# Optimization experiments

Measured on AMD Instinct MI355X. Metric: run time of the kernel, lower is better.

## Reference

```python
import jax, jax.numpy as jnp
import numpy as np

N = 100_000      # nodes (10kb Hi-C bins)
E = 3_200_000    # edges (avg degree 32)
IN = 6           # histone-mark features
HID1 = 6
HID2 = 30
HEADS = 4
NEG_SLOPE = 0.2  # PyG GATConv default LeakyReLU slope


def setup_inputs() -> dict:
    key = jax.random.key(0)
    ks = jax.random.split(key, 16)
    def glorot(k, shape, fan_in):
        return (jax.random.normal(k, shape, jnp.float32) / np.float32(np.sqrt(fan_in)))
    x = jax.random.normal(ks[0], (N, IN), jnp.float32)
    edge_index = jax.random.randint(ks[1], (2, E), 0, N, dtype=jnp.int32)
    edge_attr = jax.random.uniform(ks[2], (E,), jnp.float32)  # ignored (edge_dim=None)
    # GATConv 1: IN -> HID1, HEADS, concat=True
    w1 = glorot(ks[3], (IN, HEADS * HID1), IN)
    att_src1 = glorot(ks[4], (HEADS, HID1), HID1)
    att_dst1 = glorot(ks[5], (HEADS, HID1), HID1)
    b1 = jnp.zeros((HEADS * HID1,), jnp.float32)
    # GATConv 2: HEADS*HID1 -> HID2, HEADS, concat=False (head mean)
    w2 = glorot(ks[6], (HEADS * HID1, HEADS * HID2), HEADS * HID1)
    att_src2 = glorot(ks[7], (HEADS, HID2), HID2)
    att_dst2 = glorot(ks[8], (HEADS, HID2), HID2)
    b2 = jnp.zeros((HID2,), jnp.float32)
    # MLP head
    ffw1 = glorot(ks[9], (HID2, HID2 // 2), HID2)
    ffb1 = jnp.zeros((HID2 // 2,), jnp.float32)
    ffw2 = glorot(ks[10], (HID2 // 2, 2), HID2 // 2)
    ffb2 = jnp.zeros((2,), jnp.float32)
    return {"x": x, "edge_index": edge_index, "edge_attr": edge_attr,
            "w1": w1, "att_src1": att_src1, "att_dst1": att_dst1, "b1": b1,
            "w2": w2, "att_src2": att_src2, "att_dst2": att_dst2, "b2": b2,
            "ffw1": ffw1, "ffb1": ffb1, "ffw2": ffw2, "ffb2": ffb2}


def _leaky(z):
    return jnp.where(z > 0, z, NEG_SLOPE * z)


def _gat_conv(x, src, dst, W, a_src, a_dst, b, heads, ch, concat):
    n = x.shape[0]
    h = (x @ W).reshape(n, heads, ch)                       # [N,H,C]
    asrc = jnp.einsum('nhc,hc->nh', h, a_src)               # [N,H]
    adst = jnp.einsum('nhc,hc->nh', h, a_dst)               # [N,H]
    e = _leaky(asrc[src] + adst[dst])                       # [E,H]
    # stable segment softmax over incoming edges of each dst node
    m = jax.ops.segment_max(e, dst, num_segments=n)
    e = jnp.exp(e - m[dst])
    denom = jax.ops.segment_sum(e, dst, num_segments=n)
    alpha = e / (denom[dst] + 1e-16)                        # [E,H]
    msg = h[src] * alpha[:, :, None]                        # [E,H,C]
    out = jax.ops.segment_sum(msg, dst, num_segments=n)     # [N,H,C]
    out = out.reshape(n, heads * ch) if concat else out.mean(axis=1)
    return out + b


def reference(x, edge_index, edge_attr, w1, att_src1, att_dst1, b1,
              w2, att_src2, att_dst2, b2, ffw1, ffb1, ffw2, ffb2):
    n = x.shape[0]
    # PyG GATConv add_self_loops=True (edge_attr ignored: edge_dim=None)
    loops = jnp.arange(n, dtype=edge_index.dtype)
    ei = jnp.concatenate([edge_index, jnp.stack([loops, loops])], axis=1)
    src, dst = ei[0], ei[1]
    h = jax.nn.relu(_gat_conv(x, src, dst, w1, att_src1, att_dst1, b1, HEADS, HID1, True))
    h = jax.nn.relu(_gat_conv(h, src, dst, w2, att_src2, att_dst2, b2, HEADS, HID2, False))
    # dropout(p=0.5) is identity at inference
    h = jax.nn.relu(h @ ffw1 + ffb1)
    return h @ ffw2 + ffb2
```

## Files before the change

### kernel.cpp

```cpp
#include <hip/hip_runtime.h>

#define NEG_SLOPE 0.2f
#define NPB 128
#define MAXB 1024

__global__ void p0_count(const int* __restrict__ dst, int* __restrict__ bcnt,
                         int E, int nbuck)
{
    __shared__ int hist[MAXB];
    for (int b = threadIdx.x; b < nbuck; b += blockDim.x) hist[b] = 0;
    __syncthreads();
    int tile = blockIdx.x * 4096;
    int cnt = min(4096, E - tile);
    for (int k = threadIdx.x; k < cnt; k += blockDim.x)
        atomicAdd(&hist[dst[tile + k] >> 7], 1);
    __syncthreads();
    for (int b = threadIdx.x; b < nbuck; b += blockDim.x) {
        int v = hist[b];
        if (v) atomicAdd(&bcnt[b], v);
    }
}

__global__ void p1_scan(const int* __restrict__ bcnt, int* __restrict__ bbase,
                        int* __restrict__ bcur, int nbuck)
{
    __shared__ int sm[MAXB];
    int t = threadIdx.x;
    int v = (t < nbuck) ? bcnt[t] : 0;
    sm[t] = v;
    __syncthreads();
    for (int off = 1; off < MAXB; off <<= 1) {
        int x = (t >= off) ? sm[t - off] : 0;
        __syncthreads();
        sm[t] += x;
        __syncthreads();
    }
    if (t < nbuck) { int e = sm[t] - v; bbase[t] = e; bcur[t] = e; }
}

__global__ void p2_scatter(const int* __restrict__ src, const int* __restrict__ dst,
                           int* __restrict__ bcur, int* __restrict__ ebuf,
                           int E, int nbuck)
{
    __shared__ int hist[MAXB];
    __shared__ int base[MAXB];
    __shared__ int pk[4096];
    __shared__ unsigned short pb[4096];
    for (int b = threadIdx.x; b < nbuck; b += blockDim.x) hist[b] = 0;
    __syncthreads();
    int tile = blockIdx.x * 4096;
    int cnt = min(4096, E - tile);
    for (int k = threadIdx.x; k < cnt; k += blockDim.x) {
        int i = tile + k;
        int d = dst[i];
        int b = d >> 7;
        pk[k] = (src[i] << 7) | (d & 127);
        pb[k] = (unsigned short)b;
        atomicAdd(&hist[b], 1);
    }
    __syncthreads();
    for (int b = threadIdx.x; b < nbuck; b += blockDim.x) {
        int v = hist[b];
        base[b] = v ? atomicAdd(&bcur[b], v) : 0;
        hist[b] = 0;
    }
    __syncthreads();
    for (int k = threadIdx.x; k < cnt; k += blockDim.x) {
        int b = pb[k];
        int r = atomicAdd(&hist[b], 1);
        ebuf[base[b] + r] = pk[k];
    }
}

__global__ void p3_sort(const int* __restrict__ bbase, const int* __restrict__ bcnt,
                        const int* __restrict__ ebuf,
                        int* __restrict__ rowp, int* __restrict__ deg,
                        int* __restrict__ esrc, int N)
{
    __shared__ int hist[NPB];
    __shared__ int ls[NPB];
    int b = blockIdx.x;
    int n0 = b * NPB;
    if (threadIdx.x < NPB) hist[threadIdx.x] = 0;
    __syncthreads();
    int es = bbase[b], ec = bcnt[b];
    for (int k = threadIdx.x; k < ec; k += blockDim.x)
        atomicAdd(&hist[ebuf[es + k] & 127], 1);
    __syncthreads();
    if (threadIdx.x < NPB) ls[threadIdx.x] = hist[threadIdx.x];
    __syncthreads();
    for (int off = 1; off < NPB; off <<= 1) {
        int v = 0;
        if (threadIdx.x < NPB && threadIdx.x >= off) v = ls[threadIdx.x - off];
        __syncthreads();
        if (threadIdx.x < NPB) ls[threadIdx.x] += v;
        __syncthreads();
    }
    if (threadIdx.x < NPB) {
        int ex = ls[threadIdx.x] - hist[threadIdx.x];
        ls[threadIdx.x] = ex;
        int n = n0 + threadIdx.x;
        if (n < N) { rowp[n] = es + ex; deg[n] = hist[threadIdx.x]; }
        hist[threadIdx.x] = 0;
    }
    __syncthreads();
    for (int k = threadIdx.x; k < ec; k += blockDim.x) {
        int v = ebuf[es + k];
        int ln = v & 127;
        int r = atomicAdd(&hist[ln], 1);
        esrc[es + ls[ln] + r] = v >> 7;
    }
}

__global__ void k_fold(const float* __restrict__ W1,
                       const float* __restrict__ s1, const float* __restrict__ d1,
                       const float* __restrict__ W2,
                       const float* __restrict__ s2, const float* __restrict__ d2,
                       float* __restrict__ fold)
{
    int t = threadIdx.x;
    if (t < 24) {
        int h = t / 6, k = t % 6;
        float v = 0.f;
        for (int c = 0; c < 6; ++c) v += W1[k * 24 + h * 6 + c] * s1[h * 6 + c];
        fold[t] = v;
    } else if (t < 48) {
        int u = t - 24, h = u / 6, k = u % 6;
        float v = 0.f;
        for (int c = 0; c < 6; ++c) v += W1[k * 24 + h * 6 + c] * d1[h * 6 + c];
        fold[t] = v;
    } else if (t < 144) {
        int u = t - 48, h = u / 24, k = u % 24;
        float v = 0.f;
        for (int c = 0; c < 30; ++c) v += W2[k * 120 + h * 30 + c] * s2[h * 30 + c];
        fold[t] = v;
    } else if (t < 240) {
        int u = t - 144, h = u / 24, k = u % 24;
        float v = 0.f;
        for (int c = 0; c < 30; ++c) v += W2[k * 120 + h * 30 + c] * d2[h * 30 + c];
        fold[t] = v;
    }
}

__global__ void k1_logits(const float* __restrict__ x,
                          const float* __restrict__ fold,
                          float* __restrict__ as1, float* __restrict__ ad1, int N)
{
    int n = blockIdx.x * blockDim.x + threadIdx.x;
    if (n >= N) return;
    float xv[6];
#pragma unroll
    for (int k = 0; k < 6; ++k) xv[k] = x[n * 6 + k];
#pragma unroll
    for (int h = 0; h < 4; ++h) {
        float as = 0.f, ad = 0.f;
#pragma unroll
        for (int k = 0; k < 6; ++k) {
            as += xv[k] * fold[h * 6 + k];
            ad += xv[k] * fold[24 + h * 6 + k];
        }
        as1[n * 4 + h] = as;
        ad1[n * 4 + h] = ad;
    }
}

__global__ void k_gather1(const int* __restrict__ rowp, const int* __restrict__ deg,
                          const int* __restrict__ esrc,
                          const float* __restrict__ x,
                          const float* __restrict__ as1, const float* __restrict__ ad1,
                          const float* __restrict__ W1, const float* __restrict__ b1,
                          float* __restrict__ g1, int N)
{
    int t = blockIdx.x * blockDim.x + threadIdx.x;
    int n = t >> 2;
    if (n >= N) return;
    int h = t & 3;
    float adn = ad1[n * 4 + h];

    float e0 = as1[n * 4 + h] + adn;
    e0 = e0 > 0.f ? e0 : NEG_SLOPE * e0;
    float w = expf(e0);
    float den = w;
    float acc[6];
    {
        const float2* xp = (const float2*)(x + (size_t)n * 6);
        float2 a = xp[0], b = xp[1], c = xp[2];
        acc[0] = w * a.x; acc[1] = w * a.y; acc[2] = w * b.x;
        acc[3] = w * b.y; acc[4] = w * c.x; acc[5] = w * c.y;
    }
    int start = rowp[n], cnt = deg[n];
    for (int k = 0; k < cnt; ++k) {
        int s = esrc[start + k];
        float e = as1[s * 4 + h] + adn;
        e = e > 0.f ? e : NEG_SLOPE * e;
        w = expf(e);
        den += w;
        const float2* xp = (const float2*)(x + (size_t)s * 6);
        float2 a = xp[0], b = xp[1], c = xp[2];
        acc[0] += w * a.x; acc[1] += w * a.y; acc[2] += w * b.x;
        acc[3] += w * b.y; acc[4] += w * c.x; acc[5] += w * c.y;
    }
    float inv = 1.f / (den + 1e-16f);
    float m[6];
#pragma unroll
    for (int k = 0; k < 6; ++k) m[k] = acc[k] * inv;
#pragma unroll
    for (int c = 0; c < 6; ++c) {
        float v = b1[h * 6 + c];
#pragma unroll
        for (int k = 0; k < 6; ++k) v += m[k] * W1[k * 24 + h * 6 + c];
        g1[(size_t)n * 24 + h * 6 + c] = v > 0.f ? v : 0.f;
    }
}

__global__ void k3_logits(const float* __restrict__ g1,
                          const float* __restrict__ fold,
                          float* __restrict__ as2, float* __restrict__ ad2, int N)
{
    int n = blockIdx.x * blockDim.x + threadIdx.x;
    if (n >= N) return;
    float g[24];
    const float4* gp = (const float4*)(g1 + (size_t)n * 24);
#pragma unroll
    for (int q = 0; q < 6; ++q) {
        float4 v = gp[q];
        g[q * 4 + 0] = v.x; g[q * 4 + 1] = v.y; g[q * 4 + 2] = v.z; g[q * 4 + 3] = v.w;
    }
#pragma unroll
    for (int h = 0; h < 4; ++h) {
        float as = 0.f, ad = 0.f;
#pragma unroll
        for (int k = 0; k < 24; ++k) {
            as += g[k] * fold[48 + h * 24 + k];
            ad += g[k] * fold[144 + h * 24 + k];
        }
        as2[n * 4 + h] = as;
        ad2[n * 4 + h] = ad;
    }
}

__global__ void k_gather2(const int* __restrict__ rowp, const int* __restrict__ deg,
                          const int* __restrict__ esrc,
                          const float* __restrict__ g1,
                          const float* __restrict__ as2, const float* __restrict__ ad2,
                          const float* __restrict__ W2, const float* __restrict__ b2,
                          const float* __restrict__ fw1, const float* __restrict__ fb1,
                          const float* __restrict__ fw2, const float* __restrict__ fb2,
                          float* __restrict__ out, int N)
{
    int t = blockIdx.x * blockDim.x + threadIdx.x;
    int n = t >> 2;
    if (n >= N) return;
    int h = t & 3;
    float adn = ad2[n * 4 + h];

    float acc[24];
    float e0 = as2[n * 4 + h] + adn;
    e0 = e0 > 0.f ? e0 : NEG_SLOPE * e0;
    float w = expf(e0);
    float den = w;
    {
        const float4* gp = (const float4*)(g1 + (size_t)n * 24);
#pragma unroll
        for (int q = 0; q < 6; ++q) {
            float4 v = gp[q];
            acc[q * 4 + 0] = w * v.x; acc[q * 4 + 1] = w * v.y;
            acc[q * 4 + 2] = w * v.z; acc[q * 4 + 3] = w * v.w;
        }
    }
    int start = rowp[n], cnt = deg[n];
    for (int k = 0; k < cnt; ++k) {
        int s = esrc[start + k];
        float e = as2[s * 4 + h] + adn;
        e = e > 0.f ? e : NEG_SLOPE * e;
        w = expf(e);
        den += w;
        const float4* gp = (const float4*)(g1 + (size_t)s * 24);
#pragma unroll
        for (int q = 0; q < 6; ++q) {
            float4 v = gp[q];
            acc[q * 4 + 0] += w * v.x; acc[q * 4 + 1] += w * v.y;
            acc[q * 4 + 2] += w * v.z; acc[q * 4 + 3] += w * v.w;
        }
    }
    float inv = 1.f / (den + 1e-16f);
#pragma unroll
    for (int k = 0; k < 24; ++k) acc[k] *= inv;

    float zz[30];
#pragma unroll
    for (int c = 0; c < 30; ++c) {
        float v = 0.f;
#pragma unroll
        for (int k = 0; k < 24; ++k) v += acc[k] * W2[k * 120 + h * 30 + c];
        v += __shfl_xor(v, 1);
        v += __shfl_xor(v, 2);
        zz[c] = v;
    }
    if (h == 0) {
#pragma unroll
        for (int c = 0; c < 30; ++c) {
            float v = 0.25f * zz[c] + b2[c];
            zz[c] = v > 0.f ? v : 0.f;
        }
        float m2[15];
#pragma unroll
        for (int j = 0; j < 15; ++j) {
            float v = fb1[j];
#pragma unroll
            for (int c = 0; c < 30; ++c) v += zz[c] * fw1[c * 15 + j];
            m2[j] = v > 0.f ? v : 0.f;
        }
#pragma unroll
        for (int k = 0; k < 2; ++k) {
            float v = fb2[k];
#pragma unroll
            for (int j = 0; j < 15; ++j) v += m2[j] * fw2[j * 2 + k];
            out[(size_t)n * 2 + k] = v;
        }
    }
}

extern "C" void kernel_launch(void* const* d_in, const int* in_sizes, int n_in,
                              void* d_out, int out_size, void* d_ws, size_t ws_size,
                              hipStream_t stream)
{
    const float* x    = (const float*)d_in[0];
    const int*   ei   = (const int*)  d_in[1];
    const float* w1   = (const float*)d_in[3];
    const float* as1w = (const float*)d_in[4];
    const float* ad1w = (const float*)d_in[5];
    const float* b1   = (const float*)d_in[6];
    const float* w2   = (const float*)d_in[7];
    const float* as2w = (const float*)d_in[8];
    const float* ad2w = (const float*)d_in[9];
    const float* b2   = (const float*)d_in[10];
    const float* fw1  = (const float*)d_in[11];
    const float* fb1  = (const float*)d_in[12];
    const float* fw2  = (const float*)d_in[13];
    const float* fb2  = (const float*)d_in[14];

    const int N = in_sizes[0] / 6;
    const int E = in_sizes[1] / 2;
    const int* src = ei;
    const int* dst = ei + E;
    const int nbuck = (N + NPB - 1) / NPB;

    float* ws = (float*)d_ws;
    size_t off = 0;
    float* as1  = ws + off; off += (size_t)N * 4;
    float* ad1  = ws + off; off += (size_t)N * 4;
    float* g1   = ws + off; off += (size_t)N * 24;
    float* as2  = ws + off; off += (size_t)N * 4;
    float* ad2  = ws + off; off += (size_t)N * 4;
    float* fold = ws + off; off += 256;

    int* iw = (int*)(ws + off);
    size_t ioff = 0;
    int* bcnt  = iw + ioff; ioff += MAXB;
    int* bbase = iw + ioff; ioff += MAXB;
    int* bcur  = iw + ioff; ioff += MAXB;
    int* rowp  = iw + ioff; ioff += N;
    int* deg   = iw + ioff; ioff += N;
    int* ebuf  = iw + ioff; ioff += E;
    int* esrc  = iw + ioff; ioff += E;

    hipMemsetAsync(bcnt, 0, MAXB * sizeof(int), stream);

    const int B = 256;
    const int NB = (N + B - 1) / B;
    const int TB = (E + 4095) / 4096;
    const int QB = (N * 4 + B - 1) / B;

    k_fold    <<<1, 256, 0, stream>>>(w1, as1w, ad1w, w2, as2w, ad2w, fold);

    p0_count  <<<TB, B, 0, stream>>>(dst, bcnt, E, nbuck);
    p1_scan   <<<1, MAXB, 0, stream>>>(bcnt, bbase, bcur, nbuck);
    p2_scatter<<<TB, B, 0, stream>>>(src, dst, bcur, ebuf, E, nbuck);
    p3_sort   <<<nbuck, B, 0, stream>>>(bbase, bcnt, ebuf, rowp, deg, esrc, N);

    k1_logits <<<NB, B, 0, stream>>>(x, fold, as1, ad1, N);
    k_gather1 <<<QB, B, 0, stream>>>(rowp, deg, esrc, x, as1, ad1, w1, b1, g1, N);

    k3_logits <<<NB, B, 0, stream>>>(g1, fold, as2, ad2, N);
    k_gather2 <<<QB, B, 0, stream>>>(rowp, deg, esrc, g1, as2, ad2, w2, b2,
                                     fw1, fb1, fw2, fb2, (float*)d_out, N);
}
```

Measured before the change: 388.2 us.

## Fuse layer-2 logits into gather1, store g1 as fp16, split edges across two lanes

Layer-2 attention logits are now computed inside gather1 through cross-lane shuffles, which removes the separate k3_logits kernel and its re-read of g1. The hidden features g1 are stored as fp16, halving the bytes gathered per edge in gather2. Both gather kernels now use 8 lanes per node, each pair of lanes splitting a node's edges by parity, which doubles parallelism and shortens the serial per-node loop. The cost is fp16 rounding error in layer-2 inputs, plus extra shuffles and idle lanes in the epilogue.

```diff
diff --git a/kernel.cpp b/kernel.cpp
--- a/kernel.cpp
+++ b/kernel.cpp
@@ -1,4 +1,5 @@
 #include <hip/hip_runtime.h>
+#include <hip/hip_fp16.h>
 
 #define NEG_SLOPE 0.2f
 #define NPB 128
@@ -169,79 +170,93 @@
                           const float* __restrict__ x,
                           const float* __restrict__ as1, const float* __restrict__ ad1,
                           const float* __restrict__ W1, const float* __restrict__ b1,
-                          float* __restrict__ g1, int N)
+                          const float* __restrict__ fold,
+                          __half* __restrict__ g1h,
+                          float* __restrict__ as2, float* __restrict__ ad2, int N)
 {
     int t = blockIdx.x * blockDim.x + threadIdx.x;
-    int n = t >> 2;
+    int n = t >> 3;
     if (n >= N) return;
-    int h = t & 3;
+    int o = t & 7;
+    int h = o & 3;
+    int half = o >> 2;
     float adn = ad1[n * 4 + h];
 
-    float e0 = as1[n * 4 + h] + adn;
-    e0 = e0 > 0.f ? e0 : NEG_SLOPE * e0;
-    float w = expf(e0);
-    float den = w;
-    float acc[6];
-    {
+    float acc[6] = {0.f, 0.f, 0.f, 0.f, 0.f, 0.f};
+    float den = 0.f;
+    if (half == 0) {
+        float e0 = as1[n * 4 + h] + adn;
+        e0 = e0 > 0.f ? e0 : NEG_SLOPE * e0;
+        float w = expf(e0);
+        den = w;
         const float2* xp = (const float2*)(x + (size_t)n * 6);
         float2 a = xp[0], b = xp[1], c = xp[2];
         acc[0] = w * a.x; acc[1] = w * a.y; acc[2] = w * b.x;
         acc[3] = w * b.y; acc[4] = w * c.x; acc[5] = w * c.y;
     }
     int start = rowp[n], cnt = deg[n];
-    for (int k = 0; k < cnt; ++k) {
+    for (int k = half; k < cnt; k += 2) {
         int s = esrc[start + k];
         float e = as1[s * 4 + h] + adn;
         e = e > 0.f ? e : NEG_SLOPE * e;
-        w = expf(e);
+        float w = expf(e);
         den += w;
         const float2* xp = (const float2*)(x + (size_t)s * 6);
         float2 a = xp[0], b = xp[1], c = xp[2];
         acc[0] += w * a.x; acc[1] += w * a.y; acc[2] += w * b.x;
         acc[3] += w * b.y; acc[4] += w * c.x; acc[5] += w * c.y;
     }
+    den += __shfl_xor(den, 4);
+#pragma unroll
+    for (int k = 0; k < 6; ++k) acc[k] += __shfl_xor(acc[k], 4);
+
     float inv = 1.f / (den + 1e-16f);
     float m[6];
 #pragma unroll
     for (int k = 0; k < 6; ++k) m[k] = acc[k] * inv;
+
+    float gc[6];
 #pragma unroll
     for (int c = 0; c < 6; ++c) {
         float v = b1[h * 6 + c];
 #pragma unroll
         for (int k = 0; k < 6; ++k) v += m[k] * W1[k * 24 + h * 6 + c];
-        g1[(size_t)n * 24 + h * 6 + c] = v > 0.f ? v : 0.f;
-    }
-}
-
-__global__ void k3_logits(const float* __restrict__ g1,
-                          const float* __restrict__ fold,
-                          float* __restrict__ as2, float* __restrict__ ad2, int N)
-{
-    int n = blockIdx.x * blockDim.x + threadIdx.x;
-    if (n >= N) return;
-    float g[24];
-    const float4* gp = (const float4*)(g1 + (size_t)n * 24);
-#pragma unroll
-    for (int q = 0; q < 6; ++q) {
-        float4 v = gp[q];
-        g[q * 4 + 0] = v.x; g[q * 4 + 1] = v.y; g[q * 4 + 2] = v.z; g[q * 4 + 3] = v.w;
-    }
-#pragma unroll
-    for (int h = 0; h < 4; ++h) {
-        float as = 0.f, ad = 0.f;
-#pragma unroll
-        for (int k = 0; k < 24; ++k) {
-            as += g[k] * fold[48 + h * 24 + k];
-            ad += g[k] * fold[144 + h * 24 + k];
-        }
-        as2[n * 4 + h] = as;
-        ad2[n * 4 + h] = ad;
+        gc[c] = v > 0.f ? v : 0.f;
+    }
+    float pas[4], pad[4];
+#pragma unroll
+    for (int hh = 0; hh < 4; ++hh) {
+        float a = 0.f, d = 0.f;
+#pragma unroll
+        for (int c = 0; c < 6; ++c) {
+            a += gc[c] * fold[48 + hh * 24 + h * 6 + c];
+            d += gc[c] * fold[144 + hh * 24 + h * 6 + c];
+        }
+        pas[hh] = a; pad[hh] = d;
+    }
+#pragma unroll
+    for (int hh = 0; hh < 4; ++hh) {
+        pas[hh] += __shfl_xor(pas[hh], 1);
+        pas[hh] += __shfl_xor(pas[hh], 2);
+        pad[hh] += __shfl_xor(pad[hh], 1);
+        pad[hh] += __shfl_xor(pad[hh], 2);
+    }
+    if (half == 0) {
+        __half2 p0 = __floats2half2_rn(gc[0], gc[1]);
+        __half2 p1 = __floats2half2_rn(gc[2], gc[3]);
+        __half2 p2 = __floats2half2_rn(gc[4], gc[5]);
+        unsigned int* gp = (unsigned int*)(g1h + (size_t)n * 24 + h * 6);
+        gp[0] = *(unsigned int*)&p0;
+        gp[1] = *(unsigned int*)&p1;
+        gp[2] = *(unsigned int*)&p2;
+        as2[n * 4 + h] = pas[h];
+        ad2[n * 4 + h] = pad[h];
     }
 }
 
 __global__ void k_gather2(const int* __restrict__ rowp, const int* __restrict__ deg,
                           const int* __restrict__ esrc,
-                          const float* __restrict__ g1,
+                          const __half* __restrict__ g1h,
                           const float* __restrict__ as2, const float* __restrict__ ad2,
                           const float* __restrict__ W2, const float* __restrict__ b2,
                           const float* __restrict__ fw1, const float* __restrict__ fb1,
@@ -249,66 +264,96 @@
                           float* __restrict__ out, int N)
 {
     int t = blockIdx.x * blockDim.x + threadIdx.x;
-    int n = t >> 2;
+    int n = t >> 3;
     if (n >= N) return;
-    int h = t & 3;
+    int o = t & 7;
+    int h = o & 3;
+    int half = o >> 2;
     float adn = ad2[n * 4 + h];
 
     float acc[24];
-    float e0 = as2[n * 4 + h] + adn;
-    e0 = e0 > 0.f ? e0 : NEG_SLOPE * e0;
-    float w = expf(e0);
-    float den = w;
-    {
-        const float4* gp = (const float4*)(g1 + (size_t)n * 24);
-#pragma unroll
-        for (int q = 0; q < 6; ++q) {
-            float4 v = gp[q];
-            acc[q * 4 + 0] = w * v.x; acc[q * 4 + 1] = w * v.y;
-            acc[q * 4 + 2] = w * v.z; acc[q * 4 + 3] = w * v.w;
+#pragma unroll
+    for (int k = 0; k < 24; ++k) acc[k] = 0.f;
+    float den = 0.f;
+
+    if (half == 0) {
+        float e0 = as2[n * 4 + h] + adn;
+        e0 = e0 > 0.f ? e0 : NEG_SLOPE * e0;
+        float w = expf(e0);
+        den = w;
+        const uint4* gp = (const uint4*)(g1h + (size_t)n * 24);
+#pragma unroll
+        for (int q = 0; q < 3; ++q) {
+            uint4 u = gp[q];
+            float2 f0 = __half22float2(*(__half2*)&u.x);
+            float2 f1 = __half22float2(*(__half2*)&u.y);
+            float2 f2 = __half22float2(*(__half2*)&u.z);
+            float2 f3 = __half22float2(*(__half2*)&u.w);
+            acc[q * 8 + 0] = w * f0.x; acc[q * 8 + 1] = w * f0.y;
+            acc[q * 8 + 2] = w * f1.x; acc[q * 8 + 3] = w * f1.y;
+            acc[q * 8 + 4] = w * f2.x; acc[q * 8 + 5] = w * f2.y;
+            acc[q * 8 + 6] = w * f3.x; acc[q * 8 + 7] = w * f3.y;
         }
     }
     int start = rowp[n], cnt = deg[n];
-    for (int k = 0; k < cnt; ++k) {
+    for (int k = half; k < cnt; k += 2) {
         int s = esrc[start + k];
         float e = as2[s * 4 + h] + adn;
         e = e > 0.f ? e : NEG_SLOPE * e;
-        w = expf(e);
+        float w = expf(e);
         den += w;
-        const float4* gp = (const float4*)(g1 + (size_t)s * 24);
-#pragma unroll
-        for (int q = 0; q < 6; ++q) {
-            float4 v = gp[q];
-            acc[q * 4 + 0] += w * v.x; acc[q * 4 + 1] += w * v.y;
-            acc[q * 4 + 2] += w * v.z; acc[q * 4 + 3] += w * v.w;
-        }
-    }
+        const uint4* gp = (const uint4*)(g1h + (size_t)s * 24);
+#pragma unroll
+        for (int q = 0; q < 3; ++q) {
+            uint4 u = gp[q];
+            float2 f0 = __half22float2(*(__half2*)&u.x);
+            float2 f1 = __half22float2(*(__half2*)&u.y);
+            float2 f2 = __half22float2(*(__half2*)&u.z);
+            float2 f3 = __half22float2(*(__half2*)&u.w);
+            acc[q * 8 + 0] += w * f0.x; acc[q * 8 + 1] += w * f0.y;
+            acc[q * 8 + 2] += w * f1.x; acc[q * 8 + 3] += w * f1.y;
+            acc[q * 8 + 4] += w * f2.x; acc[q * 8 + 5] += w * f2.y;
+            acc[q * 8 + 6] += w * f3.x; acc[q * 8 + 7] += w * f3.y;
+        }
+    }
+    den += __shfl_xor(den, 4);
+#pragma unroll
+    for (int k = 0; k < 24; ++k) acc[k] += __shfl_xor(acc[k], 4);
+
     float inv = 1.f / (den + 1e-16f);
 #pragma unroll
     for (int k = 0; k < 24; ++k) acc[k] *= inv;
 
-    float zz[30];
-#pragma unroll
-    for (int c = 0; c < 30; ++c) {
+    float zz[15];
+#pragma unroll
+    for (int cc = 0; cc < 15; ++cc) {
+        int c = half * 15 + cc;
         float v = 0.f;
 #pragma unroll
         for (int k = 0; k < 24; ++k) v += acc[k] * W2[k * 120 + h * 30 + c];
         v += __shfl_xor(v, 1);
         v += __shfl_xor(v, 2);
-        zz[c] = v;
-    }
-    if (h == 0) {
-#pragma unroll
-        for (int c = 0; c < 30; ++c) {
-            float v = 0.25f * zz[c] + b2[c];
-            zz[c] = v > 0.f ? v : 0.f;
+        zz[cc] = v;
+    }
+    float zhi[15];
+#pragma unroll
+    for (int cc = 0; cc < 15; ++cc) zhi[cc] = __shfl_xor(zz[cc], 4);
+
+    if (o == 0) {
+        float z[30];
+#pragma unroll
+        for (int cc = 0; cc < 15; ++cc) {
+            float v0 = 0.25f * zz[cc] + b2[cc];
+            float v1 = 0.25f * zhi[cc] + b2[15 + cc];
+            z[cc]      = v0 > 0.f ? v0 : 0.f;
+            z[15 + cc] = v1 > 0.f ? v1 : 0.f;
         }
         float m2[15];
 #pragma unroll
         for (int j = 0; j < 15; ++j) {
             float v = fb1[j];
 #pragma unroll
-            for (int c = 0; c < 30; ++c) v += zz[c] * fw1[c * 15 + j];
+            for (int c = 0; c < 30; ++c) v += z[c] * fw1[c * 15 + j];
             m2[j] = v > 0.f ? v : 0.f;
         }
 #pragma unroll
@@ -350,10 +395,10 @@
     size_t off = 0;
     float* as1  = ws + off; off += (size_t)N * 4;
     float* ad1  = ws + off; off += (size_t)N * 4;
-    float* g1   = ws + off; off += (size_t)N * 24;
     float* as2  = ws + off; off += (size_t)N * 4;
     float* ad2  = ws + off; off += (size_t)N * 4;
     float* fold = ws + off; off += 256;
+    __half* g1h = (__half*)(ws + off); off += (size_t)N * 12;
 
     int* iw = (int*)(ws + off);
     size_t ioff = 0;
@@ -370,7 +415,7 @@
     const int B = 256;
     const int NB = (N + B - 1) / B;
     const int TB = (E + 4095) / 4096;
-    const int QB = (N * 4 + B - 1) / B;
+    const int OB = ((size_t)N * 8 + B - 1) / B;
 
     k_fold    <<<1, 256, 0, stream>>>(w1, as1w, ad1w, w2, as2w, ad2w, fold);
 
@@ -380,9 +425,9 @@
     p3_sort   <<<nbuck, B, 0, stream>>>(bbase, bcnt, ebuf, rowp, deg, esrc, N);
 
     k1_logits <<<NB, B, 0, stream>>>(x, fold, as1, ad1, N);
-    k_gather1 <<<QB, B, 0, stream>>>(rowp, deg, esrc, x, as1, ad1, w1, b1, g1, N);
-
-    k3_logits <<<NB, B, 0, stream>>>(g1, fold, as2, ad2, N);
-    k_gather2 <<<QB, B, 0, stream>>>(rowp, deg, esrc, g1, as2, ad2, w2, b2,
+    k_gather1 <<<OB, B, 0, stream>>>(rowp, deg, esrc, x, as1, ad1, w1, b1,
+                                     fold, g1h, as2, ad2, N);
+
+    k_gather2 <<<OB, B, 0, stream>>>(rowp, deg, esrc, g1h, as2, ad2, w2, b2,
                                      fw1, fb1, fw2, fb2, (float*)d_out, N);
 }
```

Result: faster. 377.6 us (-2.7%).
